# Performance work log

Hardware: AMD Instinct MI355X
Metric: run time of the kernel (lower is better)

The kernel has to match this reference:

```python
import jax, jax.numpy as jnp
import numpy as np
from jax import lax

VOCAB = 12000
EMB = 512
RNN = 512
FEATS = 4096
SEQ_LEN = 15


def setup_inputs() -> dict:
    key = jax.random.key(0)
    ks = jax.random.split(key, 10)
    B = 1024
    s = 0.05
    return {
        "img_features": jax.random.normal(ks[0], (B, FEATS), jnp.float32),
        "W_feats": jax.random.normal(ks[1], (EMB, FEATS), jnp.float32) * s,
        "b_feats": jax.random.normal(ks[2], (EMB,), jnp.float32) * s,
        "W_ih": jax.random.normal(ks[3], (4 * RNN, EMB), jnp.float32) * s,
        "W_hh": jax.random.normal(ks[4], (4 * RNN, RNN), jnp.float32) * s,
        "b_ih": jax.random.normal(ks[5], (4 * RNN,), jnp.float32) * s,
        "b_hh": jax.random.normal(ks[6], (4 * RNN,), jnp.float32) * s,
        "emb": jax.random.normal(ks[7], (VOCAB, EMB), jnp.float32) * s,
        "W_out": jax.random.normal(ks[8], (VOCAB - 2, RNN), jnp.float32) * s,
        "b_out": jax.random.normal(ks[9], (VOCAB - 2,), jnp.float32) * s,
    }


def reference(img_features, W_feats, b_feats, W_ih, W_hh, b_ih, b_hh, emb, W_out, b_out):
    B = img_features.shape[0]

    def lstm_cell(x, h, c):
        # torch.nn.LSTMCell: gates ordered i, f, g, o
        gates = x @ W_ih.T + b_ih + h @ W_hh.T + b_hh
        i, f, g, o = jnp.split(gates, 4, axis=1)
        c_new = jax.nn.sigmoid(f) * c + jax.nn.sigmoid(i) * jnp.tanh(g)
        h_new = jax.nn.sigmoid(o) * jnp.tanh(c_new)
        return h_new, c_new

    # image feature embedding + ReLU, then prime the LSTM with it
    img_vec = jax.nn.relu(img_features @ W_feats.T + b_feats)  # [B, 512]
    h = jnp.zeros((B, RNN), img_features.dtype)
    c = jnp.zeros((B, RNN), img_features.dtype)
    h, c = lstm_cell(img_vec, h, c)

    def step(carry, _):
        h, c, words = carry
        x = emb[words]                     # [B, 512] embedding lookup
        h, c = lstm_cell(x, h, c)
        logits = h @ W_out.T + b_out       # [B, VOCAB-2]
        idx = jnp.argmax(logits, axis=1).astype(jnp.int32)
        return (h, c, idx + 2), idx

    words0 = jnp.ones((B,), jnp.int32)  # START token = 1
    _, seq = lax.scan(step, (h, c, words0), None, length=SEQ_LEN)
    return seq.T  # [B, SEQ_LEN] greedy-decoded token ids
```

## Files before the change

### kernel.cpp

```cpp
#include <hip/hip_runtime.h>
#include <stdint.h>

#define BATCH  1024
#define SEQLEN 15
#define NGATE  2048
#define NVOCAB 11998
#define FEATS  4096

typedef __attribute__((ext_vector_type(8)))  short  s8v;
typedef __attribute__((ext_vector_type(16))) float  f32x16;
typedef __attribute__((ext_vector_type(8)))  unsigned short us8;

__device__ __forceinline__ unsigned short f2bf(float f) {
    unsigned u = __float_as_uint(f);
    u += 0x7FFFu + ((u >> 16) & 1u);
    return (unsigned short)(u >> 16);
}
__device__ __forceinline__ float bf2f(unsigned short h) {
    return __uint_as_float(((unsigned)h) << 16);
}
struct bfpair { unsigned short hi, lo; };
__device__ __forceinline__ bfpair split2v(float v) {
    bfpair r;
    r.hi = f2bf(v);
    r.lo = f2bf(v - bf2f(r.hi));
    return r;
}
__device__ __forceinline__ void split8(const float* __restrict__ s, us8& vh, us8& vl) {
    #pragma unroll
    for (int e = 0; e < 8; ++e) {
        bfpair q = split2v(s[e]);
        vh[e] = q.hi; vl[e] = q.lo;
    }
}

__device__ __forceinline__ void async_cp16(const void* g, void* l) {
    __builtin_amdgcn_global_load_lds(
        (const __attribute__((address_space(1))) unsigned int*)g,
        (__attribute__((address_space(3))) unsigned int*)l, 16, 0, 0);
}

__global__ void prep_wcat_blk(const float* __restrict__ W_ih, const float* __restrict__ W_hh,
                              const float* __restrict__ b_ih, const float* __restrict__ b_hh,
                              unsigned short* __restrict__ hi, unsigned short* __restrict__ lo,
                              float* __restrict__ bsum) {
    int idx = blockIdx.x * 256 + threadIdx.x;
    int kc = idx >> 11, row = idx & 2047;
    int k = kc << 3;
    const float* src = (k < 512) ? (W_ih + (size_t)row * 512 + k)
                                 : (W_hh + (size_t)row * 512 + (k - 512));
    us8 vh, vl; split8(src, vh, vl);
    *(us8*)(hi + (size_t)idx * 8) = vh;
    *(us8*)(lo + (size_t)idx * 8) = vl;
    if (idx < NGATE) bsum[idx] = b_ih[idx] + b_hh[idx];
}

__global__ void prep_blk(const float* __restrict__ src,
                         unsigned short* __restrict__ hi, unsigned short* __restrict__ lo,
                         int R, int K) {
    int row = blockIdx.x * 256 + threadIdx.x;
    if (row >= R) return;
    int kc = blockIdx.y;
    us8 vh, vl; split8(src + (size_t)row * K + (kc << 3), vh, vl);
    size_t o = ((size_t)kc * R + row) * 8;
    *(us8*)(hi + o) = vh;
    *(us8*)(lo + o) = vl;
}

template<int MODE, int MI, int NN, int PPX>
__device__ __forceinline__ void gemm_pipe(
    const unsigned short* __restrict__ Ahi, const unsigned short* __restrict__ Alo, int aRows,
    const unsigned short* __restrict__ Bhi, const unsigned short* __restrict__ Blo, int bRows,
    float* __restrict__ C, int ldc, int K,
    size_t akstride, size_t bkstride, size_t czstride,
    const float* __restrict__ bias, unsigned long long* __restrict__ packed)
{
    __shared__ short sB[2][2][4][128][8];

    int nblk, mblk, kz;
    {
        const int l = blockIdx.x;
        const int r = l & 7, q = l >> 3;
        if (NN == 94) {
            if (q < 88) { nblk = r * 11 + (q >> 3); mblk = q & 7; }
            else        { nblk = 88 + (q - 88);     mblk = r;     }
            kz = 0;
        } else {
            const int p = r * PPX + (q >> 3);
            mblk = q & 7;
            nblk = p % NN; kz = p / NN;
        }
    }

    Ahi += (size_t)kz * akstride;  Alo += (size_t)kz * akstride;
    Bhi += (size_t)kz * bkstride;  Blo += (size_t)kz * bkstride;
    C   += (size_t)kz * czstride;

    const int tid  = threadIdx.x;
    const int lane = tid & 63, wave = tid >> 6;
    const int wm = wave & 1, wn = wave >> 1;
    const int col = lane & 31, kh = lane >> 5;
    const int bm = mblk * (64 * MI), bn = nblk * 128;

    f32x16 acc[MI][2] = {};

    const int NK = K >> 5;

    #pragma unroll
    for (int p = 0; p < 4; ++p) {
        int s = p * 4 + wave;
        int arr = s >> 3, kc_l = (s >> 1) & 3, rh = s & 1;
        int brow = bn + rh * 64 + lane; if (brow > bRows - 1) brow = bRows - 1;
        size_t gb = ((size_t)kc_l * bRows + brow) * 8;
        async_cp16((arr ? Blo : Bhi) + gb, &sB[0][arr][kc_l][rh * 64][0]);
    }
    __syncthreads();

    int cur = 0;
    for (int ks = 0; ks < NK; ++ks) {
        const int kc0 = ks << 2;

        s8v ah[2][MI], al[2][MI];
        #pragma unroll
        for (int st = 0; st < 2; ++st)
            #pragma unroll
            for (int i = 0; i < MI; ++i) {
                size_t ao = ((size_t)(kc0 + 2 * st + kh) * aRows
                             + (bm + wm * 32 * MI + i * 32 + col)) * 8;
                ah[st][i] = *(const s8v*)(Ahi + ao);
                al[st][i] = *(const s8v*)(Alo + ao);
            }

        if (ks + 1 < NK) {
            const int kcn = kc0 + 4;
            #pragma unroll
            for (int p = 0; p < 4; ++p) {
                int s = p * 4 + wave;
                int arr = s >> 3, kc_l = (s >> 1) & 3, rh = s & 1;
                int brow = bn + rh * 64 + lane; if (brow > bRows - 1) brow = bRows - 1;
                size_t gb = ((size_t)(kcn + kc_l) * bRows + brow) * 8;
                async_cp16((arr ? Blo : Bhi) + gb, &sB[cur ^ 1][arr][kc_l][rh * 64][0]);
            }
        }

        #pragma unroll
        for (int st = 0; st < 2; ++st) {
            const int kl = 2 * st + kh;
            #pragma unroll
            for (int j = 0; j < 2; ++j) {
                const s8v bh = *(const s8v*)&sB[cur][0][kl][wn * 64 + j * 32 + col][0];
                const s8v bl = *(const s8v*)&sB[cur][1][kl][wn * 64 + j * 32 + col][0];
                #pragma unroll
                for (int i = 0; i < MI; ++i) {
                    acc[i][j] = __builtin_amdgcn_mfma_f32_32x32x16_bf16(ah[st][i], bh, acc[i][j], 0, 0, 0);
                    acc[i][j] = __builtin_amdgcn_mfma_f32_32x32x16_bf16(ah[st][i], bl, acc[i][j], 0, 0, 0);
                    acc[i][j] = __builtin_amdgcn_mfma_f32_32x32x16_bf16(al[st][i], bh, acc[i][j], 0, 0, 0);
                }
            }
        }

        __syncthreads();
        cur ^= 1;
    }

    if (MODE == 0) {
        #pragma unroll
        for (int i = 0; i < MI; ++i)
            #pragma unroll
            for (int rg = 0; rg < 4; ++rg)
                #pragma unroll
                for (int rr = 0; rr < 4; ++rr) {
                    int reg = rg * 4 + rr;
                    int m = bm + wm * 32 * MI + i * 32 + rr + rg * 8 + kh * 4;
                    #pragma unroll
                    for (int j = 0; j < 2; ++j) {
                        int n = bn + wn * 64 + j * 32 + col;
                        if (n < bRows) C[(size_t)m * ldc + n] = acc[i][j][reg];
                    }
                }
    } else {
        #pragma unroll
        for (int i = 0; i < MI; ++i)
            #pragma unroll
            for (int rg = 0; rg < 4; ++rg)
                #pragma unroll
                for (int rr = 0; rr < 4; ++rr) {
                    int reg = rg * 4 + rr;
                    int m = bm + wm * 32 * MI + i * 32 + rr + rg * 8 + kh * 4;
                    unsigned long long best = 0ull;
                    #pragma unroll
                    for (int j = 0; j < 2; ++j) {
                        int n = bn + wn * 64 + j * 32 + col;
                        if (n < bRows) {
                            float v = acc[i][j][reg] + bias[n];
                            unsigned int u   = __float_as_uint(v);
                            unsigned int key = (u & 0x80000000u) ? ~u : (u | 0x80000000u);
                            unsigned long long pk =
                                ((unsigned long long)key << 32) |
                                (unsigned long long)(0xFFFFFFFFu - (unsigned)n);
                            best = (pk > best) ? pk : best;
                        }
                    }
                    #pragma unroll
                    for (int sdist = 1; sdist < 32; sdist <<= 1) {
                        unsigned long long o = __shfl_xor(best, sdist, 64);
                        best = (o > best) ? o : best;
                    }
                    if (col == 0) atomicMax(&packed[m], best);
                }
    }
}

template<int PPX>
__global__ __launch_bounds__(256, 3) void k_gemm_gates(
    const unsigned short* Ahi, const unsigned short* Alo,
    const unsigned short* Bhi, const unsigned short* Blo,
    float* C, size_t aks, size_t bks, size_t czs) {
    gemm_pipe<0, 2, 16, PPX>(Ahi, Alo, 1024, Bhi, Blo, NGATE, C, NGATE, 512,
                             aks, bks, czs, nullptr, nullptr);
}
__global__ __launch_bounds__(256, 3) void k_gemm_feats(
    const unsigned short* Ahi, const unsigned short* Alo,
    const unsigned short* Bhi, const unsigned short* Blo,
    float* C) {
    gemm_pipe<0, 2, 4, 4>(Ahi, Alo, 1024, Bhi, Blo, 512, C, 512, 512,
                          (size_t)64 * 1024 * 8, (size_t)64 * 512 * 8, (size_t)1024 * 512,
                          nullptr, nullptr);
}
__global__ __launch_bounds__(256, 3) void k_logits_argmax(
    const unsigned short* __restrict__ h_hi, const unsigned short* __restrict__ h_lo,
    const unsigned short* __restrict__ wout_hi, const unsigned short* __restrict__ wout_lo,
    const float* __restrict__ bias, unsigned long long* __restrict__ packed) {
    gemm_pipe<1, 2, 94, 0>(h_hi, h_lo, 1024, wout_hi, wout_lo, NVOCAB, nullptr, 0, 512,
                           0, 0, 0, bias, packed);
}

__global__ void feats_reduce8(const float* __restrict__ part, const float* __restrict__ bias,
                              unsigned short* __restrict__ hi, unsigned short* __restrict__ lo) {
    int idx = blockIdx.x * 256 + threadIdx.x;
    int b = idx >> 6, kc = idx & 63;
    int n = kc << 3;
    float v[8];
    #pragma unroll
    for (int e = 0; e < 8; ++e) v[e] = bias[n + e];
    #pragma unroll
    for (int z = 0; z < 8; ++z) {
        const float* s = part + (size_t)z * 1024 * 512 + (size_t)b * 512 + n;
        #pragma unroll
        for (int e = 0; e < 8; ++e) v[e] += s[e];
    }
    us8 vh, vl;
    #pragma unroll
    for (int e = 0; e < 8; ++e) {
        bfpair q = split2v(fmaxf(v[e], 0.f));
        vh[e] = q.hi; vl[e] = q.lo;
    }
    size_t o = ((size_t)kc * 1024 + b) * 8;
    *(us8*)(hi + o) = vh;
    *(us8*)(lo + o) = vl;
}

template<bool PRIME>
__global__ void lstm_pw_blk(const float* __restrict__ g0, const float* __restrict__ g1,
                            const float* __restrict__ bsum, float* __restrict__ cbuf,
                            unsigned short* __restrict__ xh_hi, unsigned short* __restrict__ xh_lo,
                            unsigned long long* __restrict__ packed,
                            int* __restrict__ out, int t) {
    int idx = blockIdx.x * 256 + threadIdx.x;
    int b = idx >> 6, j8 = idx & 63;
    int j = j8 << 3;
    const float* g = g0 + (size_t)b * NGATE;
    float v[4][8];
    #pragma unroll
    for (int gt = 0; gt < 4; ++gt) {
        const float* s = g + gt * 512 + j;
        const float* bs = bsum + gt * 512 + j;
        #pragma unroll
        for (int e = 0; e < 8; ++e) v[gt][e] = s[e] + bs[e];
    }
    if (!PRIME) {
        const float* h2 = g1 + (size_t)b * NGATE;
        #pragma unroll
        for (int gt = 0; gt < 4; ++gt) {
            const float* s = h2 + gt * 512 + j;
            #pragma unroll
            for (int e = 0; e < 8; ++e) v[gt][e] += s[e];
        }
    }
    float* cb = cbuf + (size_t)b * 512 + j;
    us8 vh, vl;
    #pragma unroll
    for (int e = 0; e < 8; ++e) {
        float si = 1.f / (1.f + expf(-v[0][e]));
        float sf = 1.f / (1.f + expf(-v[1][e]));
        float tg = tanhf(v[2][e]);
        float so = 1.f / (1.f + expf(-v[3][e]));
        float cn = PRIME ? (si * tg) : (sf * cb[e] + si * tg);
        cb[e] = cn;
        bfpair q = split2v(so * tanhf(cn));
        vh[e] = q.hi; vl[e] = q.lo;
    }
    size_t o = ((size_t)(64 + j8) * 1024 + b) * 8;
    *(us8*)(xh_hi + o) = vh;
    *(us8*)(xh_lo + o) = vl;
    if (j8 == 0) {
        if (!PRIME && t > 0) {
            unsigned long long p = packed[b];
            out[b * SEQLEN + (t - 1)] = (int)(0xFFFFFFFFu - (unsigned)(p & 0xFFFFFFFFull));
        }
        packed[b] = 0ull;
    }
}

template<int FIRST>
__global__ void gather_blk(const float* __restrict__ emb,
                           const unsigned long long* __restrict__ packed,
                           unsigned short* __restrict__ xh_hi, unsigned short* __restrict__ xh_lo) {
    int idx = blockIdx.x * 256 + threadIdx.x;
    int b = idx >> 6, kc = idx & 63;
    int word = 1;
    if (!FIRST) {
        unsigned long long p = packed[b];
        word = (int)(0xFFFFFFFFu - (unsigned)(p & 0xFFFFFFFFull)) + 2;
    }
    us8 vh, vl; split8(emb + (size_t)word * 512 + (kc << 3), vh, vl);
    size_t o = ((size_t)kc * 1024 + b) * 8;
    *(us8*)(xh_hi + o) = vh;
    *(us8*)(xh_lo + o) = vl;
}

__global__ void final_out(const unsigned long long* __restrict__ packed, int* __restrict__ out) {
    int b = blockIdx.x * 256 + threadIdx.x;
    if (b < BATCH) {
        unsigned long long p = packed[b];
        out[b * SEQLEN + (SEQLEN - 1)] = (int)(0xFFFFFFFFu - (unsigned)(p & 0xFFFFFFFFull));
    }
}

extern "C" void kernel_launch(void* const* d_in, const int* in_sizes, int n_in,
                              void* d_out, int out_size, void* d_ws, size_t ws_size,
                              hipStream_t stream) {
    const float* img     = (const float*)d_in[0];
    const float* W_feats = (const float*)d_in[1];
    const float* b_feats = (const float*)d_in[2];
    const float* W_ih    = (const float*)d_in[3];
    const float* W_hh    = (const float*)d_in[4];
    const float* b_ih    = (const float*)d_in[5];
    const float* b_hh    = (const float*)d_in[6];
    const float* emb     = (const float*)d_in[7];
    const float* W_out   = (const float*)d_in[8];
    const float* b_out   = (const float*)d_in[9];
    int* out = (int*)d_out;

    const size_t WCAT_H = (size_t)128 * 2048 * 8;
    const size_t WOUT_H = (size_t)64 * NVOCAB * 8;
    const size_t XH_H   = (size_t)128 * 1024 * 8;
    const size_t IMGV_H = (size_t)64 * 1024 * 8;

    char* p = (char*)d_ws;
    unsigned short* wcat_hi = (unsigned short*)p;  p += WCAT_H * 2;
    unsigned short* wcat_lo = (unsigned short*)p;  p += WCAT_H * 2;
    unsigned short* wout_hi = (unsigned short*)p;  p += WOUT_H * 2;
    unsigned short* wout_lo = (unsigned short*)p;  p += WOUT_H * 2;
    unsigned short* xh_hi   = (unsigned short*)p;  p += XH_H * 2;
    unsigned short* xh_lo   = (unsigned short*)p;  p += XH_H * 2;
    unsigned short* imgv_hi = (unsigned short*)p;  p += IMGV_H * 2;
    unsigned short* imgv_lo = (unsigned short*)p;  p += IMGV_H * 2;
    float* cbuf             = (float*)p;           p += (size_t)1024 * 512 * 4;
    float* bsum             = (float*)p;           p += (size_t)NGATE * 4;
    unsigned long long* packed = (unsigned long long*)p;  p += (size_t)1024 * 8;
    float* gates0           = (float*)p;           p += (size_t)1024 * NGATE * 4;
    float* gates1           = (float*)p;           p += (size_t)1024 * NGATE * 4;
    unsigned short* imgb_hi = wout_hi;
    unsigned short* imgb_lo = imgb_hi + (size_t)512 * 1024 * 8;
    unsigned short* wfb_hi  = imgb_lo + (size_t)512 * 1024 * 8;
    unsigned short* wfb_lo  = wfb_hi  + (size_t)512 * 512 * 8;
    float* partials = gates0;

    prep_wcat_blk<<<1024, 256, 0, stream>>>(W_ih, W_hh, b_ih, b_hh, wcat_hi, wcat_lo, bsum);
    prep_blk<<<dim3(4, 512), 256, 0, stream>>>(img,     imgb_hi, imgb_lo, 1024, FEATS);
    prep_blk<<<dim3(2, 512), 256, 0, stream>>>(W_feats, wfb_hi,  wfb_lo,  512,  FEATS);

    k_gemm_feats<<<256, 256, 0, stream>>>(imgb_hi, imgb_lo, wfb_hi, wfb_lo, partials);
    feats_reduce8<<<256, 256, 0, stream>>>(partials, b_feats, imgv_hi, imgv_lo);

    prep_blk<<<dim3(47, 64), 256, 0, stream>>>(W_out, wout_hi, wout_lo, NVOCAB, 512);

    k_gemm_gates<2><<<128, 256, 0, stream>>>(imgv_hi, imgv_lo, wcat_hi, wcat_lo,
                                             gates0, 0, 0, 0);
    lstm_pw_blk<true><<<256, 256, 0, stream>>>(gates0, nullptr, bsum, cbuf,
                                               xh_hi, xh_lo, packed, out, 0);

    for (int t = 0; t < SEQLEN; ++t) {
        if (t == 0) gather_blk<1><<<256, 256, 0, stream>>>(emb, packed, xh_hi, xh_lo);
        else        gather_blk<0><<<256, 256, 0, stream>>>(emb, packed, xh_hi, xh_lo);
        k_gemm_gates<4><<<256, 256, 0, stream>>>(
            xh_hi, xh_lo, wcat_hi, wcat_lo, gates0,
            (size_t)64 * 1024 * 8, (size_t)64 * 2048 * 8, (size_t)1024 * NGATE);
        lstm_pw_blk<false><<<256, 256, 0, stream>>>(gates0, gates1, bsum, cbuf,
                                                    xh_hi, xh_lo, packed, out, t);
        k_logits_argmax<<<752, 256, 0, stream>>>(
            xh_hi + (size_t)64 * 1024 * 8, xh_lo + (size_t)64 * 1024 * 8,
            wout_hi, wout_lo, b_out, packed);
    }
    final_out<<<4, 256, 0, stream>>>(packed, out);
}
```

Baseline: 1.806 ms.

## Triple-buffer B tiles and prefetch A registers in the split-bf16 GEMM pipeline

The shared B tile buffer grows from two stages to three, and the next A fragments are prefetched into registers one iteration ahead. A manual vmcnt wait plus a raw barrier replaces the per-iteration __syncthreads. The K loop is fixed at 16 iterations and fully unrolled. This aims to hide global-load latency behind the MFMA work, at the cost of more registers and LDS, so launch bounds drop from 3 to 2 blocks per CU and occupancy falls.

```diff
diff --git a/kernel.cpp b/kernel.cpp
--- a/kernel.cpp
+++ b/kernel.cpp
@@ -71,11 +71,11 @@
 __device__ __forceinline__ void gemm_pipe(
     const unsigned short* __restrict__ Ahi, const unsigned short* __restrict__ Alo, int aRows,
     const unsigned short* __restrict__ Bhi, const unsigned short* __restrict__ Blo, int bRows,
-    float* __restrict__ C, int ldc, int K,
+    float* __restrict__ C, int ldc,
     size_t akstride, size_t bkstride, size_t czstride,
     const float* __restrict__ bias, unsigned long long* __restrict__ packed)
 {
-    __shared__ short sB[2][2][4][128][8];
+    __shared__ short sB[3][2][4][128][8];
 
     int nblk, mblk, kz;
     {
@@ -104,23 +104,19 @@
 
     f32x16 acc[MI][2] = {};
 
-    const int NK = K >> 5;
-
-    #pragma unroll
-    for (int p = 0; p < 4; ++p) {
-        int s = p * 4 + wave;
-        int arr = s >> 3, kc_l = (s >> 1) & 3, rh = s & 1;
-        int brow = bn + rh * 64 + lane; if (brow > bRows - 1) brow = bRows - 1;
-        size_t gb = ((size_t)kc_l * bRows + brow) * 8;
-        async_cp16((arr ? Blo : Bhi) + gb, &sB[0][arr][kc_l][rh * 64][0]);
-    }
-    __syncthreads();
-
-    int cur = 0;
-    for (int ks = 0; ks < NK; ++ks) {
-        const int kc0 = ks << 2;
-
-        s8v ah[2][MI], al[2][MI];
+    constexpr int NK = 16;
+
+    auto stage_tile = [&](int kcbase, int bufi) {
+        #pragma unroll
+        for (int p = 0; p < 4; ++p) {
+            int s = p * 4 + wave;
+            int arr = s >> 3, kc_l = (s >> 1) & 3, rh = s & 1;
+            int brow = bn + rh * 64 + lane; if (brow > bRows - 1) brow = bRows - 1;
+            size_t gb = ((size_t)(kcbase + kc_l) * bRows + brow) * 8;
+            async_cp16((arr ? Blo : Bhi) + gb, &sB[bufi][arr][kc_l][rh * 64][0]);
+        }
+    };
+    auto load_a = [&](int kc0, s8v (&ah)[2][MI], s8v (&al)[2][MI]) {
         #pragma unroll
         for (int st = 0; st < 2; ++st)
             #pragma unroll
@@ -130,37 +126,50 @@
                 ah[st][i] = *(const s8v*)(Ahi + ao);
                 al[st][i] = *(const s8v*)(Alo + ao);
             }
-
-        if (ks + 1 < NK) {
-            const int kcn = kc0 + 4;
-            #pragma unroll
-            for (int p = 0; p < 4; ++p) {
-                int s = p * 4 + wave;
-                int arr = s >> 3, kc_l = (s >> 1) & 3, rh = s & 1;
-                int brow = bn + rh * 64 + lane; if (brow > bRows - 1) brow = bRows - 1;
-                size_t gb = ((size_t)(kcn + kc_l) * bRows + brow) * 8;
-                async_cp16((arr ? Blo : Bhi) + gb, &sB[cur ^ 1][arr][kc_l][rh * 64][0]);
-            }
-        }
-
+    };
+
+    stage_tile(0, 0);
+    stage_tile(4, 1);
+    s8v ahc[2][MI], alc[2][MI], ahn[2][MI], aln[2][MI];
+    load_a(0, ahc, alc);
+
+    #pragma unroll
+    for (int t = 0; t < NK; ++t) {
+        if (t + 1 < NK) load_a((t + 1) << 2, ahn, aln);
+
+        if (t + 1 < NK) asm volatile("s_waitcnt vmcnt(16)" ::: "memory");
+        else            asm volatile("s_waitcnt vmcnt(0)"  ::: "memory");
+        __builtin_amdgcn_s_barrier();
+        __builtin_amdgcn_sched_barrier(0);
+
+        if (t + 2 < NK) stage_tile((t + 2) << 2, (t + 2) % 3);
+
+        const int bi = t % 3;
         #pragma unroll
         for (int st = 0; st < 2; ++st) {
             const int kl = 2 * st + kh;
             #pragma unroll
             for (int j = 0; j < 2; ++j) {
-                const s8v bh = *(const s8v*)&sB[cur][0][kl][wn * 64 + j * 32 + col][0];
-                const s8v bl = *(const s8v*)&sB[cur][1][kl][wn * 64 + j * 32 + col][0];
+                const s8v bh = *(const s8v*)&sB[bi][0][kl][wn * 64 + j * 32 + col][0];
+                const s8v bl = *(const s8v*)&sB[bi][1][kl][wn * 64 + j * 32 + col][0];
                 #pragma unroll
                 for (int i = 0; i < MI; ++i) {
-                    acc[i][j] = __builtin_amdgcn_mfma_f32_32x32x16_bf16(ah[st][i], bh, acc[i][j], 0, 0, 0);
-                    acc[i][j] = __builtin_amdgcn_mfma_f32_32x32x16_bf16(ah[st][i], bl, acc[i][j], 0, 0, 0);
-                    acc[i][j] = __builtin_amdgcn_mfma_f32_32x32x16_bf16(al[st][i], bh, acc[i][j], 0, 0, 0);
+                    acc[i][j] = __builtin_amdgcn_mfma_f32_32x32x16_bf16(ahc[st][i], bh, acc[i][j], 0, 0, 0);
+                    acc[i][j] = __builtin_amdgcn_mfma_f32_32x32x16_bf16(ahc[st][i], bl, acc[i][j], 0, 0, 0);
+                    acc[i][j] = __builtin_amdgcn_mfma_f32_32x32x16_bf16(alc[st][i], bh, acc[i][j], 0, 0, 0);
                 }
             }
         }
 
-        __syncthreads();
-        cur ^= 1;
+        if (t + 1 < NK) {
+            #pragma unroll
+            for (int st = 0; st < 2; ++st)
+                #pragma unroll
+                for (int i = 0; i < MI; ++i) {
+                    ahc[st][i] = ahn[st][i];
+                    alc[st][i] = aln[st][i];
+                }
+        }
     }
 
     if (MODE == 0) {
@@ -212,26 +221,26 @@
 }
 
 template<int PPX>
-__global__ __launch_bounds__(256, 3) void k_gemm_gates(
+__global__ __launch_bounds__(256, 2) void k_gemm_gates(
     const unsigned short* Ahi, const unsigned short* Alo,
     const unsigned short* Bhi, const unsigned short* Blo,
     float* C, size_t aks, size_t bks, size_t czs) {
-    gemm_pipe<0, 2, 16, PPX>(Ahi, Alo, 1024, Bhi, Blo, NGATE, C, NGATE, 512,
+    gemm_pipe<0, 2, 16, PPX>(Ahi, Alo, 1024, Bhi, Blo, NGATE, C, NGATE,
                              aks, bks, czs, nullptr, nullptr);
 }
-__global__ __launch_bounds__(256, 3) void k_gemm_feats(
+__global__ __launch_bounds__(256, 2) void k_gemm_feats(
     const unsigned short* Ahi, const unsigned short* Alo,
     const unsigned short* Bhi, const unsigned short* Blo,
     float* C) {
-    gemm_pipe<0, 2, 4, 4>(Ahi, Alo, 1024, Bhi, Blo, 512, C, 512, 512,
+    gemm_pipe<0, 2, 4, 4>(Ahi, Alo, 1024, Bhi, Blo, 512, C, 512,
                           (size_t)64 * 1024 * 8, (size_t)64 * 512 * 8, (size_t)1024 * 512,
                           nullptr, nullptr);
 }
-__global__ __launch_bounds__(256, 3) void k_logits_argmax(
+__global__ __launch_bounds__(256, 2) void k_logits_argmax(
     const unsigned short* __restrict__ h_hi, const unsigned short* __restrict__ h_lo,
     const unsigned short* __restrict__ wout_hi, const unsigned short* __restrict__ wout_lo,
     const float* __restrict__ bias, unsigned long long* __restrict__ packed) {
-    gemm_pipe<1, 2, 94, 0>(h_hi, h_lo, 1024, wout_hi, wout_lo, NVOCAB, nullptr, 0, 512,
+    gemm_pipe<1, 2, 94, 0>(h_hi, h_lo, 1024, wout_hi, wout_lo, NVOCAB, nullptr, 0,
                            0, 0, 0, bias, packed);
 }
 
```

Measured after the change: 1.896 ms. 1.05x slower.
